# Performance work log

Measured on AMD Instinct MI355X. Metric: run time of the kernel, lower is better.

The kernel has to match this reference:

```python
import jax, jax.numpy as jnp
import numpy as np

D_MODEL = 256
D_STATE = 2
BATCH = 8
SEQ = 8192


def setup_inputs() -> dict:
    key = jax.random.key(0)
    ks = jax.random.split(key, 8)
    s = 1.0 / np.sqrt(D_STATE)
    x = jax.random.normal(ks[0], (BATCH, SEQ, D_MODEL), dtype=jnp.float32)
    # stable range so exp(cumsum) stays finite at T=8192 (see notes)
    log_a_mag = -jax.random.uniform(ks[1], (D_MODEL, D_STATE), jnp.float32, 1e-5, 1e-3)
    a_phase = jax.random.uniform(ks[2], (D_MODEL, D_STATE), jnp.float32, 0.0, 2.0 * np.pi)
    B_re = jax.random.normal(ks[3], (D_MODEL, D_STATE), jnp.float32) * s
    B_im = jax.random.normal(ks[4], (D_MODEL, D_STATE), jnp.float32) * s
    C_re = jax.random.normal(ks[5], (D_MODEL, D_STATE), jnp.float32) * s
    C_im = jax.random.normal(ks[6], (D_MODEL, D_STATE), jnp.float32) * s
    D_diag = jnp.ones((D_MODEL,), jnp.float32)
    return dict(x=x, log_a_mag=log_a_mag, a_phase=a_phase, B_re=B_re, B_im=B_im,
                C_re=C_re, C_im=C_im, D_diag=D_diag)


def reference(x, log_a_mag, a_phase, B_re, B_im, C_re, C_im, D_diag):
    # x: (B, T, D); params: (D, S)
    Bsz, T, D = x.shape
    S = log_a_mag.shape[1]
    # cumulative complex log-decay along time, shape (D, S, T)
    cum_r = jnp.cumsum(jnp.broadcast_to(log_a_mag[:, :, None], (D, S, T)), axis=-1)
    cum_i = jnp.cumsum(jnp.broadcast_to(a_phase[:, :, None], (D, S, T)), axis=-1)
    x_t = jnp.swapaxes(x, 1, 2)                      # (B, D, T)
    Bu_r = B_re[None, :, :, None] * x_t[:, :, None, :]   # (B, D, S, T)
    Bu_i = B_im[None, :, :, None] * x_t[:, :, None, :]
    # exp(-cum_log_a): descale inputs
    en = jnp.exp(-cum_r)
    enr = en * jnp.cos(-cum_i)
    eni = en * jnp.sin(-cum_i)
    sr = enr * Bu_r - eni * Bu_i
    si = enr * Bu_i + eni * Bu_r
    csr = jnp.cumsum(sr, axis=-1)
    csi = jnp.cumsum(si, axis=-1)
    # exp(+cum_log_a): rescale prefix sums -> hidden states h (B, D, S, T)
    ec = jnp.exp(cum_r)
    ecr = ec * jnp.cos(cum_i)
    eci = ec * jnp.sin(cum_i)
    h_r = ecr * csr - eci * csi
    h_i = ecr * csi + eci * csr
    # output: Re(C . h) summed over state + skip D*x
    y = jnp.einsum('bdst,ds->bdt', h_r, C_re) - jnp.einsum('bdst,ds->bdt', h_i, C_im)
    y = jnp.swapaxes(y, 1, 2) + D_diag * x           # (B, T, D)
    return y
```

## Files before the change

### kernel.cpp

```cpp
#include <hip/hip_runtime.h>
#include <math.h>

#define BATCH  8
#define SEQ    8192
#define DMODEL 256
#define DSTATE 2
#define CHUNKS 256
#define CLEN   32
#define CPAD   1040

typedef float floatx4 __attribute__((ext_vector_type(4)));


__global__ void ssm_chunk_state(const float* __restrict__ x,
                                const float* __restrict__ lam,
                                const float* __restrict__ aph,
                                const float* __restrict__ Bre,
                                const float* __restrict__ Bim,
                                float* __restrict__ E) {
    const int lane = threadIdx.x;
    const int bid  = blockIdx.x;
    const int b = bid >> 8;
    const int c = bid & (CHUNKS - 1);
    const int d0 = lane * 4;

    float ar[4][2], ai[4][2], br[4][2], bi[4][2];
#pragma unroll
    for (int j = 0; j < 4; ++j) {
        const int d = d0 + j;
#pragma unroll
        for (int s = 0; s < 2; ++s) {
            const float lm = lam[d * 2 + s];
            const float ph = aph[d * 2 + s];
            const float m  = expf(lm);
            ar[j][s] = m * cosf(ph);
            ai[j][s] = m * sinf(ph);
            br[j][s] = Bre[d * 2 + s];
            bi[j][s] = Bim[d * 2 + s];
        }
    }

    float hr[4][2] = {}, hi[4][2] = {};
    const float* xp = x + ((size_t)b * SEQ + (size_t)c * CLEN) * DMODEL + d0;
#pragma unroll 4
    for (int t = 0; t < CLEN; ++t) {
        const float4 xv = *reinterpret_cast<const float4*>(xp + (size_t)t * DMODEL);
        const float xj[4] = {xv.x, xv.y, xv.z, xv.w};
#pragma unroll
        for (int j = 0; j < 4; ++j) {
#pragma unroll
            for (int s = 0; s < 2; ++s) {
                const float nr = fmaf(ar[j][s], hr[j][s],
                                 fmaf(-ai[j][s], hi[j][s], br[j][s] * xj[j]));
                const float ni = fmaf(ar[j][s], hi[j][s],
                                 fmaf( ai[j][s], hr[j][s], bi[j][s] * xj[j]));
                hr[j][s] = nr;
                hi[j][s] = ni;
            }
        }
    }

    float* ep = E + (size_t)bid * CPAD + lane * 16;
#pragma unroll
    for (int j = 0; j < 4; ++j) {
        float4 v;
        v.x = hr[j][0]; v.y = hi[j][0];
        v.z = hr[j][1]; v.w = hi[j][1];
        reinterpret_cast<float4*>(ep)[j] = v;
    }
}

__global__ void ssm_chunk_scan(const float* __restrict__ E,
                               float* __restrict__ Hin,
                               const float* __restrict__ lam,
                               const float* __restrict__ aph) {
    const int lane = threadIdx.x & 63;
    const int g = blockIdx.x * 4 + (threadIdx.x >> 6);
    const int b = g >> 9;
    const int r = g & 511;
    const int d = (r >> 3) * 4 + ((r >> 1) & 3);
    const int s = r & 1;

    const double lm = (double)lam[d * 2 + s];
    const double ph = (double)aph[d * 2 + s];
    const double mL = exp(lm * (double)CLEN);
    const double pL = ph * (double)CLEN;
    const float Ar = (float)(mL * cos(pL));
    const float Ai = (float)(mL * sin(pL));

    const size_t base = (size_t)b * CHUNKS * CPAD + (size_t)r * 2;

    float2 e[4];
#pragma unroll
    for (int i = 0; i < 4; ++i) {
        const int cc = lane * 4 + i;
        e[i] = *reinterpret_cast<const float2*>(E + base + (size_t)cc * CPAD);
    }

    float vr = e[0].x, vi = e[0].y;
#pragma unroll
    for (int i = 1; i < 4; ++i) {
        const float nr = fmaf(Ar, vr, fmaf(-Ai, vi, e[i].x));
        const float ni = fmaf(Ar, vi, fmaf( Ai, vr, e[i].y));
        vr = nr; vi = ni;
    }

#pragma unroll
    for (int st = 0; st < 6; ++st) {
        const int k = 1 << st;
        const double n = (double)CLEN * 4.0 * (double)k;
        const double mm = exp(lm * n);
        const double pp = ph * n;
        const float Wr = (float)(mm * cos(pp));
        const float Wi = (float)(mm * sin(pp));
        const float ur = __shfl_up(vr, (unsigned)k);
        const float ui = __shfl_up(vi, (unsigned)k);
        if (lane >= k) {
            vr = fmaf(Wr, ur, fmaf(-Wi, ui, vr));
            vi = fmaf(Wr, ui, fmaf( Wi, ur, vi));
        }
    }

    float pr = __shfl_up(vr, 1);
    float pi = __shfl_up(vi, 1);
    if (lane == 0) { pr = 0.f; pi = 0.f; }

#pragma unroll
    for (int i = 0; i < 4; ++i) {
        const int cc = lane * 4 + i;
        *reinterpret_cast<float2*>(Hin + base + (size_t)cc * CPAD) =
            make_float2(pr, pi);
        const float nr = fmaf(Ar, pr, fmaf(-Ai, pi, e[i].x));
        const float ni = fmaf(Ar, pi, fmaf( Ai, pr, e[i].y));
        pr = nr; pi = ni;
    }
}

__global__ void ssm_output(const float* __restrict__ x,
                           const float* __restrict__ lam,
                           const float* __restrict__ aph,
                           const float* __restrict__ Bre,
                           const float* __restrict__ Bim,
                           const float* __restrict__ Cre,
                           const float* __restrict__ Cim,
                           const float* __restrict__ Dd,
                           const float* __restrict__ Hin,
                           float* __restrict__ y) {
    const int lane = threadIdx.x;
    const int bid  = blockIdx.x;
    const int b = bid >> 8;
    const int c = bid & (CHUNKS - 1);
    const int d0 = lane * 4;

    float ar[4][2], ai[4][2], br[4][2], bi[4][2], cr[4][2], ci[4][2], dd[4];
#pragma unroll
    for (int j = 0; j < 4; ++j) {
        const int d = d0 + j;
        dd[j] = Dd[d];
#pragma unroll
        for (int s = 0; s < 2; ++s) {
            const float lm = lam[d * 2 + s];
            const float ph = aph[d * 2 + s];
            const float m  = expf(lm);
            ar[j][s] = m * cosf(ph);
            ai[j][s] = m * sinf(ph);
            br[j][s] = Bre[d * 2 + s];
            bi[j][s] = Bim[d * 2 + s];
            cr[j][s] = Cre[d * 2 + s];
            ci[j][s] = Cim[d * 2 + s];
        }
    }

    float hr[4][2], hi[4][2];
    const float* hp = Hin + (size_t)bid * CPAD + lane * 16;
#pragma unroll
    for (int j = 0; j < 4; ++j) {
        const float4 v = reinterpret_cast<const float4*>(hp)[j];
        hr[j][0] = v.x; hi[j][0] = v.y;
        hr[j][1] = v.z; hi[j][1] = v.w;
    }

    const size_t tbase = ((size_t)b * SEQ + (size_t)c * CLEN) * DMODEL + d0;
    const float* xp = x + tbase;
    float* yp = y + tbase;
#pragma unroll 4
    for (int t = 0; t < CLEN; ++t) {
        const float4 xv = *reinterpret_cast<const float4*>(xp + (size_t)t * DMODEL);
        const float xj[4] = {xv.x, xv.y, xv.z, xv.w};
        float yj[4];
#pragma unroll
        for (int j = 0; j < 4; ++j) {
            float acc = dd[j] * xj[j];
#pragma unroll
            for (int s = 0; s < 2; ++s) {
                const float nr = fmaf(ar[j][s], hr[j][s],
                                 fmaf(-ai[j][s], hi[j][s], br[j][s] * xj[j]));
                const float ni = fmaf(ar[j][s], hi[j][s],
                                 fmaf( ai[j][s], hr[j][s], bi[j][s] * xj[j]));
                hr[j][s] = nr;
                hi[j][s] = ni;
                acc = fmaf(cr[j][s], nr, acc);
                acc = fmaf(-ci[j][s], ni, acc);
            }
            yj[j] = acc;
        }
        floatx4 yv;
        yv.x = yj[0]; yv.y = yj[1]; yv.z = yj[2]; yv.w = yj[3];
        __builtin_nontemporal_store(yv,
            reinterpret_cast<floatx4*>(yp + (size_t)t * DMODEL));
    }
}

extern "C" void kernel_launch(void* const* d_in, const int* in_sizes, int n_in,
                              void* d_out, int out_size, void* d_ws, size_t ws_size,
                              hipStream_t stream) {
    const float* x   = (const float*)d_in[0];
    const float* lam = (const float*)d_in[1];
    const float* aph = (const float*)d_in[2];
    const float* Bre = (const float*)d_in[3];
    const float* Bim = (const float*)d_in[4];
    const float* Cre = (const float*)d_in[5];
    const float* Cim = (const float*)d_in[6];
    const float* Dd  = (const float*)d_in[7];
    float* yo = (float*)d_out;

    float* E   = (float*)d_ws;
    float* Hin = E + (size_t)BATCH * CHUNKS * CPAD;

    ssm_chunk_state<<<BATCH * CHUNKS, 64, 0, stream>>>(x, lam, aph, Bre, Bim, E);
    ssm_chunk_scan<<<(BATCH * 512) / 4, 256, 0, stream>>>(E, Hin, lam, aph);
    ssm_output<<<BATCH * CHUNKS, 64, 0, stream>>>(x, lam, aph, Bre, Bim,
                                                  Cre, Cim, Dd, Hin, yo);
}
```

Baseline: 168.4 us.

## Halve chunk length, pack four chunks per block, square twiddles in scan

Chunk length drops from 32 to 16, so there are 512 chunks per batch. The state and output kernels now run 256-thread blocks, with each wave handling one chunk. This shortens the serial recurrence per thread and puts more waves in flight. The scan kernel handles 8 chunks per lane and builds its power twiddles by repeated complex squaring in double precision instead of calling exp/cos/sin at every step. In exchange, the intermediate E/Hin buffers double in size, and repeated squaring may add a little rounding error.

```diff
diff --git a/kernel.cpp b/kernel.cpp
--- a/kernel.cpp
+++ b/kernel.cpp
@@ -5,24 +5,26 @@
 #define SEQ    8192
 #define DMODEL 256
 #define DSTATE 2
-#define CHUNKS 256
-#define CLEN   32
+#define CHUNKS 512
+#define CLEN   16
 #define CPAD   1040
 
 typedef float floatx4 __attribute__((ext_vector_type(4)));
 
 
-__global__ void ssm_chunk_state(const float* __restrict__ x,
-                                const float* __restrict__ lam,
-                                const float* __restrict__ aph,
-                                const float* __restrict__ Bre,
-                                const float* __restrict__ Bim,
-                                float* __restrict__ E) {
-    const int lane = threadIdx.x;
+__global__ __launch_bounds__(256, 4)
+void ssm_chunk_state(const float* __restrict__ x,
+                     const float* __restrict__ lam,
+                     const float* __restrict__ aph,
+                     const float* __restrict__ Bre,
+                     const float* __restrict__ Bim,
+                     float* __restrict__ E) {
+    const int lane = threadIdx.x & 63;
+    const int w    = threadIdx.x >> 6;
     const int bid  = blockIdx.x;
-    const int b = bid >> 8;
-    const int c = bid & (CHUNKS - 1);
-    const int d0 = lane * 4;
+    const int b    = bid >> 7;
+    const int c    = ((bid & 127) << 2) + w;
+    const int d0   = lane * 4;
 
     float ar[4][2], ai[4][2], br[4][2], bi[4][2];
 #pragma unroll
@@ -60,7 +62,7 @@
         }
     }
 
-    float* ep = E + (size_t)bid * CPAD + lane * 16;
+    float* ep = E + ((size_t)b * CHUNKS + c) * CPAD + lane * 16;
 #pragma unroll
     for (int j = 0; j < 4; ++j) {
         float4 v;
@@ -70,10 +72,11 @@
     }
 }
 
-__global__ void ssm_chunk_scan(const float* __restrict__ E,
-                               float* __restrict__ Hin,
-                               const float* __restrict__ lam,
-                               const float* __restrict__ aph) {
+__global__ __launch_bounds__(256)
+void ssm_chunk_scan(const float* __restrict__ E,
+                    float* __restrict__ Hin,
+                    const float* __restrict__ lam,
+                    const float* __restrict__ aph) {
     const int lane = threadIdx.x & 63;
     const int g = blockIdx.x * 4 + (threadIdx.x >> 6);
     const int b = g >> 9;
@@ -85,40 +88,49 @@
     const double ph = (double)aph[d * 2 + s];
     const double mL = exp(lm * (double)CLEN);
     const double pL = ph * (double)CLEN;
-    const float Ar = (float)(mL * cos(pL));
-    const float Ai = (float)(mL * sin(pL));
+    double wr = mL * cos(pL);
+    double wi = mL * sin(pL);
+    const float Ar = (float)wr;
+    const float Ai = (float)wi;
 
     const size_t base = (size_t)b * CHUNKS * CPAD + (size_t)r * 2;
 
-    float2 e[4];
-#pragma unroll
-    for (int i = 0; i < 4; ++i) {
-        const int cc = lane * 4 + i;
+    float2 e[8];
+#pragma unroll
+    for (int i = 0; i < 8; ++i) {
+        const int cc = lane * 8 + i;
         e[i] = *reinterpret_cast<const float2*>(E + base + (size_t)cc * CPAD);
     }
 
     float vr = e[0].x, vi = e[0].y;
 #pragma unroll
-    for (int i = 1; i < 4; ++i) {
+    for (int i = 1; i < 8; ++i) {
         const float nr = fmaf(Ar, vr, fmaf(-Ai, vi, e[i].x));
         const float ni = fmaf(Ar, vi, fmaf( Ai, vr, e[i].y));
         vr = nr; vi = ni;
     }
 
 #pragma unroll
+    for (int q = 0; q < 3; ++q) {
+        const double tq = wr * wr - wi * wi;
+        wi = 2.0 * wr * wi;
+        wr = tq;
+    }
+
+#pragma unroll
     for (int st = 0; st < 6; ++st) {
         const int k = 1 << st;
-        const double n = (double)CLEN * 4.0 * (double)k;
-        const double mm = exp(lm * n);
-        const double pp = ph * n;
-        const float Wr = (float)(mm * cos(pp));
-        const float Wi = (float)(mm * sin(pp));
+        const float Wr = (float)wr;
+        const float Wi = (float)wi;
         const float ur = __shfl_up(vr, (unsigned)k);
         const float ui = __shfl_up(vi, (unsigned)k);
         if (lane >= k) {
             vr = fmaf(Wr, ur, fmaf(-Wi, ui, vr));
             vi = fmaf(Wr, ui, fmaf( Wi, ur, vi));
         }
+        const double tq = wr * wr - wi * wi;
+        wi = 2.0 * wr * wi;
+        wr = tq;
     }
 
     float pr = __shfl_up(vr, 1);
@@ -126,8 +138,8 @@
     if (lane == 0) { pr = 0.f; pi = 0.f; }
 
 #pragma unroll
-    for (int i = 0; i < 4; ++i) {
-        const int cc = lane * 4 + i;
+    for (int i = 0; i < 8; ++i) {
+        const int cc = lane * 8 + i;
         *reinterpret_cast<float2*>(Hin + base + (size_t)cc * CPAD) =
             make_float2(pr, pi);
         const float nr = fmaf(Ar, pr, fmaf(-Ai, pi, e[i].x));
@@ -136,21 +148,23 @@
     }
 }
 
-__global__ void ssm_output(const float* __restrict__ x,
-                           const float* __restrict__ lam,
-                           const float* __restrict__ aph,
-                           const float* __restrict__ Bre,
-                           const float* __restrict__ Bim,
-                           const float* __restrict__ Cre,
-                           const float* __restrict__ Cim,
-                           const float* __restrict__ Dd,
-                           const float* __restrict__ Hin,
-                           float* __restrict__ y) {
-    const int lane = threadIdx.x;
+__global__ __launch_bounds__(256, 4)
+void ssm_output(const float* __restrict__ x,
+                const float* __restrict__ lam,
+                const float* __restrict__ aph,
+                const float* __restrict__ Bre,
+                const float* __restrict__ Bim,
+                const float* __restrict__ Cre,
+                const float* __restrict__ Cim,
+                const float* __restrict__ Dd,
+                const float* __restrict__ Hin,
+                float* __restrict__ y) {
+    const int lane = threadIdx.x & 63;
+    const int w    = threadIdx.x >> 6;
     const int bid  = blockIdx.x;
-    const int b = bid >> 8;
-    const int c = bid & (CHUNKS - 1);
-    const int d0 = lane * 4;
+    const int b    = bid >> 7;
+    const int c    = ((bid & 127) << 2) + w;
+    const int d0   = lane * 4;
 
     float ar[4][2], ai[4][2], br[4][2], bi[4][2], cr[4][2], ci[4][2], dd[4];
 #pragma unroll
@@ -172,7 +186,7 @@
     }
 
     float hr[4][2], hi[4][2];
-    const float* hp = Hin + (size_t)bid * CPAD + lane * 16;
+    const float* hp = Hin + ((size_t)b * CHUNKS + c) * CPAD + lane * 16;
 #pragma unroll
     for (int j = 0; j < 4; ++j) {
         const float4 v = reinterpret_cast<const float4*>(hp)[j];
@@ -227,8 +241,8 @@
     float* E   = (float*)d_ws;
     float* Hin = E + (size_t)BATCH * CHUNKS * CPAD;
 
-    ssm_chunk_state<<<BATCH * CHUNKS, 64, 0, stream>>>(x, lam, aph, Bre, Bim, E);
+    ssm_chunk_state<<<BATCH * CHUNKS / 4, 256, 0, stream>>>(x, lam, aph, Bre, Bim, E);
     ssm_chunk_scan<<<(BATCH * 512) / 4, 256, 0, stream>>>(E, Hin, lam, aph);
-    ssm_output<<<BATCH * CHUNKS, 64, 0, stream>>>(x, lam, aph, Bre, Bim,
-                                                  Cre, Cim, Dd, Hin, yo);
-}
+    ssm_output<<<BATCH * CHUNKS / 4, 256, 0, stream>>>(x, lam, aph, Bre, Bim,
+                                                       Cre, Cim, Dd, Hin, yo);
+}
```

Result: slower. 200.2 us (+18.8%).
